# Optimization experiments

Hardware: AMD Instinct MI355X
Metric: run time of the kernel (lower is better)

## Reference

```python
import jax, jax.numpy as jnp
import numpy as np
from jax import lax

DILATIONS = (1, 2, 4)
K = 3        # kernel_size
HORIZON = 6


def _gcn(x, src, dst, W, b, n):
    # PyG GCNConv with self-loops: D^{-1/2}(A+I)D^{-1/2} X W + b
    xw = x @ W                                                # [N,H]
    e = src.shape[0]
    deg = 1.0 + jax.ops.segment_sum(jnp.ones((e,), x.dtype), dst, num_segments=n)
    dinv = lax.rsqrt(deg)                                     # [N]
    msg = xw[src] * (dinv[src] * dinv[dst])[:, None]          # [E,H]
    agg = jax.ops.segment_sum(msg, dst, num_segments=n)       # [N,H]
    return agg + xw * (dinv * dinv)[:, None] + b


def _cell(x, src, dst, win, gcn_w, gcn_b, conv_w, conv_b, proj_w, proj_b):
    n = x.shape[0]
    hg = jax.nn.relu(_gcn(x, src, dst, gcn_w, gcn_b, n))      # [N,H]
    tcn_in = jnp.concatenate([win[:, 1:], hg[:, None]], axis=1)  # [N,K,H]
    hin = jnp.transpose(tcn_in, (0, 2, 1))                    # [N,H,K]
    outs = []
    for i, d in enumerate(DILATIONS):
        p = (K - 1) * d // 2
        y = lax.conv_general_dilated(hin, conv_w[i], (1,), [(p, p)],
                                     rhs_dilation=(d,),
                                     dimension_numbers=('NCH', 'OIH', 'NCH'))
        outs.append(y[:, :, -1] + conv_b[i])                  # last temporal position, [N,H]
    h_new = jnp.concatenate(outs, axis=1) @ proj_w.T + proj_b  # [N,H]
    new_win = jnp.concatenate([win[:, 1:], h_new[:, None]], axis=1)
    return h_new, new_win


def reference(x_seq, edge_index_seq, edge_attr_seq, mask_seq, id_seq,
              gcn_w, gcn_b, conv_w, conv_b, proj_w, proj_b, head_w, head_b):
    T, N, _ = x_seq.shape
    H = gcn_w.shape[1]
    win0 = jnp.zeros((N, K, H), x_seq.dtype)

    def enc_step(win, inp):
        x_t, ei_t = inp
        _, win = _cell(x_t, ei_t[0], ei_t[1], win,
                       gcn_w, gcn_b, conv_w, conv_b, proj_w, proj_b)
        return win, None

    win, _ = lax.scan(enc_step, win0, (x_seq, edge_index_seq))

    src, dst = edge_index_seq[-1, 0], edge_index_seq[-1, 1]

    def dec_step(carry, _):
        win, inp = carry
        h_new, win = _cell(inp, src, dst, win,
                           gcn_w, gcn_b, conv_w, conv_b, proj_w, proj_b)
        y = h_new @ head_w.T + head_b                          # [N,C]
        return (win, y), y

    _, preds = lax.scan(dec_step, (win, x_seq[-1]), None, length=HORIZON)
    return preds  # [horizon, N, out_channels]


def setup_inputs() -> dict:
    T, N, F, E, H, C = 12, 20000, 16, 320000, 128, 16
    key = jax.random.key(0)
    ks = jax.random.split(key, 12)
    return {
        'x_seq': jax.random.normal(ks[0], (T, N, F), jnp.float32),
        'edge_index_seq': jax.random.randint(ks[1], (T, 2, E), 0, N, jnp.int64),
        'edge_attr_seq': jax.random.normal(ks[2], (T, E, 1), jnp.float32),
        'mask_seq': jnp.ones((T, N), jnp.bool_),
        'id_seq': jnp.tile(jnp.arange(N, dtype=jnp.int32)[None], (T, 1)),
        'gcn_w': jax.random.normal(ks[3], (F, H), jnp.float32) * 0.1,
        'gcn_b': jnp.zeros((H,), jnp.float32),
        'conv_w': jax.random.normal(ks[4], (3, H, H, K), jnp.float32) * 0.05,
        'conv_b': jnp.zeros((3, H), jnp.float32),
        'proj_w': jax.random.normal(ks[5], (H, 3 * H), jnp.float32) * 0.05,
        'proj_b': jnp.zeros((H,), jnp.float32),
        'head_w': jax.random.normal(ks[6], (C, H), jnp.float32) * 0.05,
        'head_b': jnp.zeros((C,), jnp.float32),
    }
```

## Files before the change

### kernel.cpp

```cpp
#include <hip/hip_runtime.h>

#define NN 20000
#define NP 20032
#define EE 320000
#define TT 12
#define HH 128
#define FF 16
#define CC 16
#define HOR 6

#define NB 313
#define WPT 84
#define CHE 3812

#define NBLK 79

typedef __attribute__((ext_vector_type(8))) short short8;
typedef __attribute__((ext_vector_type(4))) float f32x4;

__device__ __forceinline__ float blo(unsigned int u) {
    union { float f; unsigned int i; } v; v.i = u << 16; return v.f;
}
__device__ __forceinline__ float bhi(unsigned int u) {
    union { float f; unsigned int i; } v; v.i = u & 0xffff0000u; return v.f;
}
__device__ __forceinline__ unsigned short f2b(float f) {
    union { float f; unsigned int i; } v; v.f = f;
    unsigned int x = v.i;
    return (unsigned short)((x + 0x7fffu + ((x >> 16) & 1u)) >> 16);
}
__device__ __forceinline__ unsigned int pck(float lo, float hi) {
    return ((unsigned int)f2b(hi) << 16) | f2b(lo);
}
__device__ __forceinline__ void addrow(float* acc, uint4 r) {
    acc[0] += blo(r.x); acc[1] += bhi(r.x);
    acc[2] += blo(r.y); acc[3] += bhi(r.y);
    acc[4] += blo(r.z); acc[5] += bhi(r.z);
    acc[6] += blo(r.w); acc[7] += bhi(r.w);
}

__global__ void k_zero(int* p, int n) {
    int i = blockIdx.x * 256 + threadIdx.x;
    if (i < n) p[i] = 0;
}

__global__ __launch_bounds__(512) void k_binA(const int* __restrict__ ei,
                                              int* __restrict__ gData,
                                              int* __restrict__ pcnt,
                                              int* __restrict__ pofs) {
    int wg = blockIdx.x;
    int t = wg / WPT, w = wg - t * WPT;
    __shared__ int lcnt[NB];
    __shared__ int sm[512];
    __shared__ __align__(16) int elist[CHE];
    int tid = threadIdx.x;
    for (int i = tid; i < NB; i += 512) lcnt[i] = 0;
    __syncthreads();
    int e0 = w * CHE, e1 = min(EE, e0 + CHE);
    int total = e1 - e0;
    const int* si = ei + (size_t)t * 2 * EE;
    const int* di = si + EE;
    int eA = e0 + tid * 4, eB = eA + 2048;
    bool hA = eA < e1, hB = eB < e1;
    int sA[4], dA[4], pA[4], sB[4], dB[4], pB[4];
    if (hA) {
        int4 s4 = *(const int4*)(si + eA);
        int4 d4 = *(const int4*)(di + eA);
        sA[0] = s4.x; sA[1] = s4.y; sA[2] = s4.z; sA[3] = s4.w;
        dA[0] = d4.x; dA[1] = d4.y; dA[2] = d4.z; dA[3] = d4.w;
    }
    if (hB) {
        int4 s4 = *(const int4*)(si + eB);
        int4 d4 = *(const int4*)(di + eB);
        sB[0] = s4.x; sB[1] = s4.y; sB[2] = s4.z; sB[3] = s4.w;
        dB[0] = d4.x; dB[1] = d4.y; dB[2] = d4.z; dB[3] = d4.w;
    }
    if (hA) {
#pragma unroll
        for (int k = 0; k < 4; k++) pA[k] = atomicAdd(&lcnt[dA[k] >> 6], 1);
    }
    if (hB) {
#pragma unroll
        for (int k = 0; k < 4; k++) pB[k] = atomicAdd(&lcnt[dB[k] >> 6], 1);
    }
    __syncthreads();
    sm[tid] = (tid < NB) ? lcnt[tid] : 0;
    __syncthreads();
    for (int off = 1; off < 512; off <<= 1) {
        int u = (tid >= off) ? sm[tid - off] : 0;
        __syncthreads();
        sm[tid] += u;
        __syncthreads();
    }
    if (tid < NB) {
        int v = lcnt[tid];
        int ex = sm[tid] - v;
        size_t o = (size_t)(t * WPT + w) * NB + tid;
        pcnt[o] = v;
        pofs[o] = ex;
        sm[tid] = ex;
    }
    __syncthreads();
    if (hA) {
#pragma unroll
        for (int k = 0; k < 4; k++) {
            int b = dA[k] >> 6;
            elist[sm[b] + pA[k]] = ((dA[k] & 63) << 16) | sA[k];
        }
    }
    if (hB) {
#pragma unroll
        for (int k = 0; k < 4; k++) {
            int b = dB[k] >> 6;
            elist[sm[b] + pB[k]] = ((dB[k] & 63) << 16) | sB[k];
        }
    }
    __syncthreads();
    int* gOut = gData + (size_t)(t * WPT + w) * CHE;
    for (int i = tid * 4; i < total; i += 2048)
        *(int4*)(gOut + i) = *(const int4*)&elist[i];
}

__global__ __launch_bounds__(512) void k_bscan2(const int* __restrict__ pcnt,
                                                int* __restrict__ bbase,
                                                int* __restrict__ rowptr) {
    int t = blockIdx.x, tid = threadIdx.x;
    __shared__ int sm[512];
    int v = 0;
    if (tid < NB)
        for (int w = 0; w < WPT; w++) v += pcnt[(size_t)(t * WPT + w) * NB + tid];
    sm[tid] = v;
    __syncthreads();
    for (int off = 1; off < 512; off <<= 1) {
        int u = (tid >= off) ? sm[tid - off] : 0;
        __syncthreads();
        sm[tid] += u;
        __syncthreads();
    }
    if (tid < NB) bbase[t * NB + tid] = sm[tid] - v;
    if (tid == 511) rowptr[(size_t)t * (NN + 1) + NN] = sm[511];
}

__global__ __launch_bounds__(256) void k_placeB(const int* __restrict__ gData,
                                                const int* __restrict__ pcnt,
                                                const int* __restrict__ pofs,
                                                const int* __restrict__ bbase,
                                                int* __restrict__ rowptr,
                                                float* __restrict__ dinv,
                                                unsigned short* __restrict__ csr) {
    int t = blockIdx.x / NB, b = blockIdx.x - t * NB;
    int tid = threadIdx.x;
    __shared__ int scnt[WPT], sofs[WPT], cofs[WPT + 1];
    __shared__ int elist[2048];
    __shared__ int cnt64[64], lofs[64], place[64];
    if (tid < WPT) {
        size_t o = (size_t)(t * WPT + tid) * NB + b;
        scnt[tid] = pcnt[o];
        sofs[tid] = pofs[o];
    }
    if (tid < 64) cnt64[tid] = 0;
    __syncthreads();
    if (tid == 0) {
        int s = 0;
        for (int w = 0; w < WPT; w++) { cofs[w] = s; s += scnt[w]; }
        cofs[WPT] = s;
    }
    __syncthreads();
    int total = cofs[WPT];
    int wv = tid >> 6, lane = tid & 63;
    for (int w = wv; w < WPT; w += 4) {
        int c = scnt[w], o = cofs[w];
        const int* sp = gData + (size_t)(t * WPT + w) * CHE + sofs[w];
        for (int i = lane; i < c; i += 64) elist[o + i] = sp[i];
    }
    __syncthreads();
    for (int i = tid; i < total; i += 256) atomicAdd(&cnt64[elist[i] >> 16], 1);
    __syncthreads();
    if (tid == 0) {
        int s = 0;
        for (int j = 0; j < 64; j++) { lofs[j] = s; place[j] = s; s += cnt64[j]; }
    }
    __syncthreads();
    int base = bbase[t * NB + b];
    int n = b * 64 + tid;
    if (tid < 64 && n < NN) {
        rowptr[(size_t)t * (NN + 1) + n] = base + lofs[tid];
        dinv[(size_t)t * NN + n] = rsqrtf(1.0f + (float)cnt64[tid]);
    }
    unsigned short* cbase = csr + (size_t)t * EE + base;
    for (int i = tid; i < total; i += 256) {
        int en = elist[i];
        int r = atomicAdd(&place[en >> 16], 1);
        cbase[r] = (unsigned short)(en & 0xffff);
    }
}

__global__ void k_count(const int* __restrict__ ei, int* __restrict__ cnt) {
    int idx = blockIdx.x * 256 + threadIdx.x;
    if (idx >= TT * EE) return;
    int t = idx / EE, e = idx - t * EE;
    int d = ei[t * 2 * EE + EE + e];
    atomicAdd(&cnt[t * NN + d], 1);
}

__global__ void k_dinvF(const int* __restrict__ cnt, float* __restrict__ dinv) {
    int idx = blockIdx.x * 256 + threadIdx.x;
    if (idx >= TT * NN) return;
    dinv[idx] = 1.0f / sqrtf(1.0f + (float)cnt[idx]);
}

__global__ void k_scan(const int* __restrict__ cnt, int* __restrict__ rowptr, int* __restrict__ wofs) {
    int t = blockIdx.x;
    const int* c = cnt + t * NN;
    int* rp = rowptr + t * (NN + 1);
    int* wo = wofs + t * NN;
    __shared__ int sums[1024];
    int tid = threadIdx.x;
    const int CH2 = 20;
    int base = tid * CH2;
    int loc[CH2];
    int s = 0;
    for (int i = 0; i < CH2; i++) { int ix = base + i; int v = (ix < NN) ? c[ix] : 0; loc[i] = s; s += v; }
    sums[tid] = s;
    __syncthreads();
    for (int off = 1; off < 1024; off <<= 1) {
        int v = (tid >= off) ? sums[tid - off] : 0;
        __syncthreads();
        sums[tid] += v;
        __syncthreads();
    }
    int excl = (tid > 0) ? sums[tid - 1] : 0;
    for (int i = 0; i < CH2; i++) {
        int ix = base + i;
        if (ix < NN) { int e = excl + loc[i]; rp[ix] = e; wo[ix] = e; }
    }
    if (tid == 1023) rp[NN] = sums[1023];
}

__global__ void k_place(const int* __restrict__ ei, int* __restrict__ wofs,
                        unsigned short* __restrict__ csr) {
    int idx = blockIdx.x * 256 + threadIdx.x;
    if (idx >= TT * EE) return;
    int t = idx / EE, e = idx - t * EE;
    int s = ei[t * 2 * EE + e];
    int d = ei[t * 2 * EE + EE + e];
    int pos = atomicAdd(&wofs[t * NN + d], 1);
    csr[t * EE + pos] = (unsigned short)s;
}

__global__ void k_wprepB(const float* __restrict__ cw, const float* __restrict__ pw,
                         const float* __restrict__ cb, const float* __restrict__ pb,
                         unsigned short* __restrict__ Bpk, float* __restrict__ Bf32,
                         float* __restrict__ bias) {
    int idx = blockIdx.x * 256 + threadIdx.x;
    if (blockIdx.x == 192) {
        int h = threadIdx.x;
        if (h < HH) {
            float m = pb[h];
            for (int d = 0; d < 3; d++)
                for (int o = 0; o < HH; o++)
                    m += cb[d * HH + o] * pw[h * 384 + d * HH + o];
            bias[h] = m;
        }
        return;
    }
    if (idx >= 384 * HH) return;
    int kk = idx / HH, h = idx - kk * HH;
    float m = 0.f;
    if (kk < 128) {
        int i = kk;
        for (int o = 0; o < HH; o++)
            m += cw[((1 * HH + o) * HH + i) * 3 + 0] * pw[h * 384 + 128 + o];
    } else if (kk < 256) {
        int i = kk - 128;
        for (int o = 0; o < HH; o++)
            m += cw[((0 * HH + o) * HH + i) * 3 + 0] * pw[h * 384 + o];
    } else {
        int i = kk - 256;
        for (int d = 0; d < 3; d++)
            for (int o = 0; o < HH; o++)
                m += cw[((d * HH + o) * HH + i) * 3 + 1] * pw[h * 384 + d * HH + o];
    }
    Bf32[kk * HH + h] = m;
    int ki = kk >> 5, r = kk & 31, q = r >> 3, j = r & 7, nt = h >> 4, ln = q * 16 + (h & 15);
    Bpk[(size_t)((ki * 8 + nt) * 64 + ln) * 8 + j] = f2b(m);
}

__global__ __launch_bounds__(256) void k_packP(const float* __restrict__ Bf32,
                                               const float* __restrict__ biasT,
                                               unsigned short* __restrict__ Bpk2,
                                               float* __restrict__ biasP) {
    int gidx = blockIdx.x * 256 + threadIdx.x;
    if (gidx < 16 * 16 * 64 * 8) {
        int j = gidx & 7, ln = (gidx >> 3) & 63, nt = (gidx >> 9) & 15, kb = gidx >> 13;
        int q = ln >> 4;
        int kk = (kb & 3) * 32 + q * 8 + j;
        int c = nt * 16 + (ln & 15);
        int s = c >> 7, h = c & 127;
        int g = kb >> 2;
        const float* M2 = Bf32;
        const float* M1 = Bf32 + 128 * HH;
        const float* Mh = Bf32 + 256 * HH;
        float v = 0.f;
        if (g == 0) {
            if (s == 0) v = M2[kk * HH + h];
            else { for (int o = 0; o < HH; o++) v += M2[kk * HH + o] * M1[o * HH + h]; }
        } else if (g == 1) {
            if (s == 0) v = M1[kk * HH + h];
            else {
                v = M2[kk * HH + h];
                for (int o = 0; o < HH; o++) v += M1[kk * HH + o] * M1[o * HH + h];
            }
        } else if (g == 2) {
            if (s == 0) v = Mh[kk * HH + h];
            else { for (int o = 0; o < HH; o++) v += Mh[kk * HH + o] * M1[o * HH + h]; }
        } else {
            v = (s == 0) ? 0.f : Mh[kk * HH + h];
        }
        Bpk2[gidx] = f2b(v);
    } else if (gidx < 16 * 16 * 64 * 8 + 256) {
        int c = gidx - 16 * 16 * 64 * 8;
        if (c < 128) biasP[c] = biasT[c];
        else {
            int h = c & 127;
            float v = biasT[h];
            const float* M1 = Bf32 + 128 * HH;
            for (int o = 0; o < HH; o++) v += biasT[o] * M1[o * HH + h];
            biasP[c] = v;
        }
    }
}

__global__ void k_xs(const float* __restrict__ x, const float* __restrict__ dinv,
                     unsigned short* __restrict__ xs) {
    int idx = blockIdx.x * 256 + threadIdx.x;
    if (idx >= TT * NN) return;
    float dn = dinv[idx];
    const float4* xr = (const float4*)(x + (size_t)idx * FF);
    unsigned int res[8];
#pragma unroll
    for (int k = 0; k < 4; k++) {
        float4 v = xr[k];
        res[2 * k]     = pck(v.x * dn, v.y * dn);
        res[2 * k + 1] = pck(v.z * dn, v.w * dn);
    }
    uint4* dst = (uint4*)(xs + (size_t)idx * FF);
    dst[0] = *(uint4*)(res);
    dst[1] = *(uint4*)(res + 4);
}

__global__ __launch_bounds__(256) void k_aggX(const unsigned short* __restrict__ xsA,
                                              const unsigned short* __restrict__ csrA,
                                              const int* __restrict__ rpA,
                                              const float* __restrict__ dinvA,
                                              float* __restrict__ zA) {
    int b = blockIdx.x;
    int g = b / NBLK, nb = b - g * NBLK;
    int n = nb * 256 + threadIdx.x;
    if (n >= NN) return;
    const unsigned short* xs = xsA + (size_t)g * NN * FF;
    const unsigned short* csr = csrA + (size_t)g * EE;
    const int* rp = rpA + (size_t)g * (NN + 1);
    float acc[16];
    {
        const uint4* sp = (const uint4*)(xs + (size_t)n * FF);
        uint4 a = sp[0], b4 = sp[1];
        acc[0] = blo(a.x);  acc[1] = bhi(a.x);  acc[2] = blo(a.y);  acc[3] = bhi(a.y);
        acc[4] = blo(a.z);  acc[5] = bhi(a.z);  acc[6] = blo(a.w);  acc[7] = bhi(a.w);
        acc[8] = blo(b4.x); acc[9] = bhi(b4.x); acc[10] = blo(b4.y); acc[11] = bhi(b4.y);
        acc[12] = blo(b4.z); acc[13] = bhi(b4.z); acc[14] = blo(b4.w); acc[15] = bhi(b4.w);
    }
    int j0 = rp[n], j1 = rp[n + 1];
    int j = j0;
    for (; j + 1 < j1; j += 2) {
        int s0 = csr[j], s1 = csr[j + 1];
        const uint4* p0 = (const uint4*)(xs + (size_t)s0 * FF);
        const uint4* p1 = (const uint4*)(xs + (size_t)s1 * FF);
        uint4 a0 = p0[0], a1 = p0[1], b0 = p1[0], b1 = p1[1];
        addrow(acc, a0); addrow(acc + 8, a1);
        addrow(acc, b0); addrow(acc + 8, b1);
    }
    if (j < j1) {
        const uint4* p0 = (const uint4*)(xs + (size_t)csr[j] * FF);
        uint4 a0 = p0[0], a1 = p0[1];
        addrow(acc, a0); addrow(acc + 8, a1);
    }
    float dn = dinvA[(size_t)g * NN + n];
    float4* zo = (float4*)(zA + (size_t)g * NP * FF + (size_t)n * FF);
#pragma unroll
    for (int k = 0; k < 4; k++)
        zo[k] = make_float4(acc[4 * k] * dn, acc[4 * k + 1] * dn,
                            acc[4 * k + 2] * dn, acc[4 * k + 3] * dn);
}

__device__ __forceinline__ void hg_frag(const float* zsh, const float* Wg, const float* gbs,
                                        int mr, int q, short8* hgf) {
    float zr[16];
    {
        const float4* zp = (const float4*)(zsh + mr * FF);
        float4 z0 = zp[0], z1 = zp[1], z2 = zp[2], z3 = zp[3];
        zr[0] = z0.x; zr[1] = z0.y; zr[2] = z0.z; zr[3] = z0.w;
        zr[4] = z1.x; zr[5] = z1.y; zr[6] = z1.z; zr[7] = z1.w;
        zr[8] = z2.x; zr[9] = z2.y; zr[10] = z2.z; zr[11] = z2.w;
        zr[12] = z3.x; zr[13] = z3.y; zr[14] = z3.z; zr[15] = z3.w;
    }
#pragma unroll
    for (int k2 = 0; k2 < 4; k2++) {
        float s[8];
#pragma unroll
        for (int c = 0; c < 8; c++) s[c] = gbs[k2 * 32 + q * 8 + c];
#pragma unroll
        for (int f = 0; f < 16; f++) {
            const float4* wp = (const float4*)(Wg + f * HH + k2 * 32 + q * 8);
            float4 w0 = wp[0], w1 = wp[1];
            float zf = zr[f];
            s[0] += zf * w0.x; s[1] += zf * w0.y; s[2] += zf * w0.z; s[3] += zf * w0.w;
            s[4] += zf * w1.x; s[5] += zf * w1.y; s[6] += zf * w1.z; s[7] += zf * w1.w;
        }
#pragma unroll
        for (int c = 0; c < 8; c++) hgf[k2][c] = (short)f2b(fmaxf(s[c], 0.f));
    }
}

__global__ __launch_bounds__(256, 4) void k_gemm2(const unsigned short* __restrict__ a0,
                                                  const unsigned short* __restrict__ a1,
                                                  const float* __restrict__ zA,
                                                  const float* __restrict__ zB,
                                                  const float* __restrict__ gw,
                                                  const float* __restrict__ gb,
                                                  const unsigned short* __restrict__ Bpk2,
                                                  const float* __restrict__ biasP,
                                                  unsigned short* __restrict__ out0,
                                                  unsigned short* __restrict__ out1) {
    __shared__ float Wg[FF * HH];
    __shared__ float zshA[16 * FF], zshB[16 * FF];
    __shared__ float gbs[HH];
    __shared__ float bps[256];
    __shared__ __align__(16) unsigned short hgA[16 * 136], hgB[16 * 136];
    __shared__ __align__(16) unsigned short csh[16 * 264];
    int tid = threadIdx.x;
    int wid = tid >> 6, lane = tid & 63;
    int m0b = blockIdx.x * 16;
    int mr = lane & 15, q = lane >> 4;
    for (int i = tid; i < FF * HH; i += 256) Wg[i] = gw[i];
    if (tid < 16 * FF) {
        zshA[tid] = zA[(size_t)m0b * FF + tid];
        zshB[tid] = zB[(size_t)m0b * FF + tid];
    }
    if (tid < HH) gbs[tid] = gb[tid];
    bps[tid] = biasP[tid];
    __syncthreads();
    if (wid == 0) {
        short8 hgf[4];
        hg_frag(zshA, Wg, gbs, mr, q, hgf);
#pragma unroll
        for (int k2 = 0; k2 < 4; k2++)
            *(short8*)&hgA[mr * 136 + k2 * 32 + q * 8] = hgf[k2];
    } else if (wid == 1) {
        short8 hgf[4];
        hg_frag(zshB, Wg, gbs, mr, q, hgf);
#pragma unroll
        for (int k2 = 0; k2 < 4; k2++)
            *(short8*)&hgB[mr * 136 + k2 * 32 + q * 8] = hgf[k2];
    }
    __syncthreads();
    int nt0 = wid * 4;
    f32x4 acc[4];
#pragma unroll
    for (int j = 0; j < 4; j++) acc[j] = (f32x4){0.f, 0.f, 0.f, 0.f};
#pragma unroll
    for (int kb = 0; kb < 12; kb++) {
        short8 bf[4];
#pragma unroll
        for (int j = 0; j < 4; j++)
            bf[j] = *(const short8*)(Bpk2 + (size_t)((kb * 16 + nt0 + j) * 64 + lane) * 8);
        short8 af;
        if (kb < 4)
            af = *(const short8*)(a0 + (size_t)(m0b + mr) * HH + kb * 32 + q * 8);
        else if (kb < 8)
            af = *(const short8*)(a1 + (size_t)(m0b + mr) * HH + (kb - 4) * 32 + q * 8);
        else
            af = *(const short8*)&hgA[mr * 136 + (kb - 8) * 32 + q * 8];
#pragma unroll
        for (int j = 0; j < 4; j++)
            acc[j] = __builtin_amdgcn_mfma_f32_16x16x32_bf16(af, bf[j], acc[j], 0, 0, 0);
    }
    if (wid >= 2) {
#pragma unroll
        for (int k2 = 0; k2 < 4; k2++) {
            int kb = 12 + k2;
            short8 bf[4];
#pragma unroll
            for (int j = 0; j < 4; j++)
                bf[j] = *(const short8*)(Bpk2 + (size_t)((kb * 16 + nt0 + j) * 64 + lane) * 8);
            short8 af = *(const short8*)&hgB[mr * 136 + k2 * 32 + q * 8];
#pragma unroll
            for (int j = 0; j < 4; j++)
                acc[j] = __builtin_amdgcn_mfma_f32_16x16x32_bf16(af, bf[j], acc[j], 0, 0, 0);
        }
    }
#pragma unroll
    for (int j = 0; j < 4; j++) {
        int c = (nt0 + j) * 16 + mr;
        float bv = bps[c];
#pragma unroll
        for (int r = 0; r < 4; r++)
            csh[(q * 4 + r) * 264 + c] = f2b(acc[j][r] + bv);
    }
    __syncthreads();
#pragma unroll
    for (int i = 0; i < 2; i++) {
        int idx = i * 256 + tid;
        int row = idx >> 5, c8 = (idx & 31) * 8;
        short8 v = *(const short8*)&csh[row * 264 + c8];
        if (c8 < 128) *(short8*)(out0 + (size_t)(m0b + row) * HH + c8) = v;
        else          *(short8*)(out1 + (size_t)(m0b + row) * HH + (c8 - 128)) = v;
    }
}

__global__ __launch_bounds__(256, 3) void k_gemmF2(const unsigned short* __restrict__ a0,
                                                   const unsigned short* __restrict__ a1,
                                                   const float* __restrict__ zt, int gather,
                                                   const float* __restrict__ gw,
                                                   const float* __restrict__ gb,
                                                   const unsigned short* __restrict__ Bpk,
                                                   const float* __restrict__ bias,
                                                   unsigned short* __restrict__ out,
                                                   const float* __restrict__ hw,
                                                   const float* __restrict__ hbv,
                                                   const float* __restrict__ dinvN,
                                                   const int* __restrict__ rp,
                                                   const unsigned short* __restrict__ csr,
                                                   unsigned short* __restrict__ xsD,
                                                   float* __restrict__ yout) {
    __shared__ float Wg[FF * HH];
    __shared__ float Whs[CC * 132];
    __shared__ float gbs[HH], biasS[HH], hbS[CC];
    __shared__ float zsh[16 * FF];
    __shared__ __align__(16) unsigned short hgD[16 * 136];
    __shared__ unsigned short hsh[16 * 136];
    __shared__ float ysh[16 * 17];
    int tid = threadIdx.x;
    int wid = tid >> 6, lane = tid & 63;
    int m0b = blockIdx.x * 16;
    int mr = lane & 15, q = lane >> 4;
    for (int i = tid; i < FF * HH; i += 256) {
        Wg[i] = gw[i];
        Whs[(i >> 7) * 132 + (i & 127)] = hw[i];
    }
    if (tid < HH) { gbs[tid] = gb[tid]; biasS[tid] = bias[tid]; }
    if (tid < CC) hbS[tid] = hbv[tid];
    if (!gather) {
        if (tid < 16 * FF) zsh[tid] = zt[(size_t)m0b * FF + tid];
    } else {
        int r = tid >> 4, p = tid & 15, half = p & 1, eo = p >> 1;
        int n = m0b + r;
        float a[8];
#pragma unroll
        for (int k = 0; k < 8; k++) a[k] = 0.f;
        if (n < NN) {
            int j0 = rp[n], j1 = rp[n + 1];
            for (int j = j0 + eo; j < j1; j += 8) {
                int s = csr[j];
                uint4 v = *(const uint4*)(xsD + (size_t)s * FF + half * 8);
                addrow(a, v);
            }
        }
#pragma unroll
        for (int k = 0; k < 8; k++) {
            a[k] += __shfl_xor(a[k], 2);
            a[k] += __shfl_xor(a[k], 4);
            a[k] += __shfl_xor(a[k], 8);
        }
        if (n < NN && eo == 0) {
            uint4 sv = *(const uint4*)(xsD + (size_t)n * FF + half * 8);
            addrow(a, sv);
            float dn = dinvN[n];
#pragma unroll
            for (int k = 0; k < 8; k++) zsh[r * FF + half * 8 + k] = a[k] * dn;
        }
    }
    __syncthreads();
    if (wid == 0) {
        short8 hgf[4];
        hg_frag(zsh, Wg, gbs, mr, q, hgf);
#pragma unroll
        for (int k2 = 0; k2 < 4; k2++)
            *(short8*)&hgD[mr * 136 + k2 * 32 + q * 8] = hgf[k2];
    }
    __syncthreads();
    int nt0 = wid * 2;
    f32x4 acc[2];
#pragma unroll
    for (int j = 0; j < 2; j++) acc[j] = (f32x4){0.f, 0.f, 0.f, 0.f};
#pragma unroll
    for (int ki = 0; ki < 12; ki++) {
        short8 bf[2];
#pragma unroll
        for (int j = 0; j < 2; j++)
            bf[j] = *(const short8*)(Bpk + (size_t)((ki * 8 + nt0 + j) * 64 + lane) * 8);
        short8 af;
        if (ki < 4)
            af = *(const short8*)(a0 + (size_t)(m0b + mr) * HH + ki * 32 + q * 8);
        else if (ki < 8)
            af = *(const short8*)(a1 + (size_t)(m0b + mr) * HH + (ki - 4) * 32 + q * 8);
        else
            af = *(const short8*)&hgD[mr * 136 + (ki - 8) * 32 + q * 8];
#pragma unroll
        for (int j = 0; j < 2; j++)
            acc[j] = __builtin_amdgcn_mfma_f32_16x16x32_bf16(af, bf[j], acc[j], 0, 0, 0);
    }
#pragma unroll
    for (int j = 0; j < 2; j++) {
        int feat = (nt0 + j) * 16 + mr;
        float bv = biasS[feat];
#pragma unroll
        for (int r = 0; r < 4; r++)
            hsh[(q * 4 + r) * 136 + feat] = f2b(acc[j][r] + bv);
    }
    __syncthreads();
    {
        int row = tid >> 4, c8 = (tid & 15) * 8;
        *(short8*)(out + (size_t)(m0b + row) * HH + c8) =
            *(const short8*)&hsh[row * 136 + c8];
    }
    {
        int r = tid >> 4, c = tid & 15;
        float y = hbS[c];
        for (int k = 0; k < HH; k++)
            y += blo((unsigned int)hsh[r * 136 + k]) * Whs[c * 132 + k];
        ysh[r * 17 + c] = y;
        int gn = m0b + r;
        if (gn < NN) yout[(size_t)gn * CC + c] = y;
    }
    __syncthreads();
    if (tid < 16) {
        int gn = m0b + tid;
        if (gn < NN) {
            float dn = dinvN[gn];
            unsigned int res[8];
#pragma unroll
            for (int k = 0; k < 8; k++)
                res[k] = pck(ysh[tid * 17 + 2 * k] * dn, ysh[tid * 17 + 2 * k + 1] * dn);
            uint4* dst = (uint4*)(xsD + (size_t)gn * FF);
            dst[0] = *(uint4*)(res);
            dst[1] = *(uint4*)(res + 4);
        }
    }
}

extern "C" void kernel_launch(void* const* d_in, const int* in_sizes, int n_in,
                              void* d_out, int out_size, void* d_ws, size_t ws_size,
                              hipStream_t stream) {
    const float* x_seq  = (const float*)d_in[0];
    const int*   ei     = (const int*)d_in[1];
    const float* gcn_w  = (const float*)d_in[5];
    const float* gcn_b  = (const float*)d_in[6];
    const float* conv_w = (const float*)d_in[7];
    const float* conv_b = (const float*)d_in[8];
    const float* proj_w = (const float*)d_in[9];
    const float* proj_b = (const float*)d_in[10];
    const float* head_w = (const float*)d_in[11];
    const float* head_b = (const float*)d_in[12];
    float* outp = (float*)d_out;

    char* ws = (char*)d_ws;
    size_t off = 0;
    auto alloc = [&](size_t bytes) { void* p = ws + off; off += (bytes + 255) & ~(size_t)255; return p; };
    float*          dinv   = (float*)alloc((size_t)TT * NN * 4);
    int*            rowptr = (int*)alloc((size_t)TT * (NN + 1) * 4);
    unsigned short* csr    = (unsigned short*)alloc((size_t)TT * EE * 2);
    unsigned short* hb0    = (unsigned short*)alloc((size_t)NP * HH * 2);
    unsigned short* hb1    = (unsigned short*)alloc((size_t)NP * HH * 2);
    unsigned short* hb2    = (unsigned short*)alloc((size_t)NP * HH * 2);
    unsigned short* hb3    = (unsigned short*)alloc((size_t)NP * HH * 2);
    unsigned short* xsD    = (unsigned short*)alloc((size_t)NP * FF * 2);
    unsigned short* Bpk    = (unsigned short*)alloc((size_t)384 * HH * 2);
    float*          Bf32   = (float*)alloc((size_t)384 * HH * 4);
    float*          biasT  = (float*)alloc(HH * 4);
    unsigned short* Bpk2   = (unsigned short*)alloc((size_t)16 * 16 * 64 * 8 * 2);
    float*          biasP  = (float*)alloc(256 * 4);
    size_t tb = off;
    unsigned short* xs12 = (unsigned short*)alloc((size_t)TT * NN * FF * 2);
    float*          z12  = (float*)alloc((size_t)TT * NP * FF * 4);
    size_t compute_end = off;
    off = tb;
    int* gData = (int*)alloc((size_t)TT * WPT * CHE * 4);
    int* pcnt  = (int*)alloc((size_t)TT * WPT * NB * 4);
    int* pofs  = (int*)alloc((size_t)TT * WPT * NB * 4);
    int* bbase = (int*)alloc((size_t)TT * NB * 4);
    size_t csr_end = off;
    bool fastcsr = (csr_end <= ws_size && compute_end <= ws_size);

    k_zero<<<(NP * HH + 255) / 256, 256, 0, stream>>>((int*)hb2, NP * HH);

    if (fastcsr) {
        k_binA<<<TT * WPT, 512, 0, stream>>>(ei, gData, pcnt, pofs);
        k_bscan2<<<TT, 512, 0, stream>>>(pcnt, bbase, rowptr);
        k_placeB<<<TT * NB, 256, 0, stream>>>(gData, pcnt, pofs, bbase, rowptr, dinv, csr);
    } else {
        off = tb;
        int* cnt  = (int*)alloc((size_t)TT * NN * 4);
        int* wofs = (int*)alloc((size_t)TT * NN * 4);
        k_zero<<<(TT * NN + 255) / 256, 256, 0, stream>>>(cnt, TT * NN);
        k_count<<<(TT * EE + 255) / 256, 256, 0, stream>>>(ei, cnt);
        k_dinvF<<<(TT * NN + 255) / 256, 256, 0, stream>>>(cnt, dinv);
        k_scan<<<TT, 1024, 0, stream>>>(cnt, rowptr, wofs);
        k_place<<<(TT * EE + 255) / 256, 256, 0, stream>>>(ei, wofs, csr);
    }

    k_wprepB<<<193, 256, 0, stream>>>(conv_w, proj_w, conv_b, proj_b, Bpk, Bf32, biasT);
    k_packP<<<(16 * 16 * 64 * 8 + 256 + 255) / 256, 256, 0, stream>>>(Bf32, biasT, Bpk2, biasP);

    k_xs<<<(TT * NN + 255) / 256, 256, 0, stream>>>(x_seq, dinv, xs12);
    k_aggX<<<TT * NBLK, 256, 0, stream>>>(xs12, csr, rowptr, dinv, z12);

    unsigned short* hbuf[4] = {hb0, hb1, hb2, hb3};
    for (int t = 0; t < TT; t += 2) {
        k_gemm2<<<NP / 16, 256, 0, stream>>>(hbuf[(t + 2) & 3], hbuf[(t + 3) & 3],
                                             z12 + (size_t)t * NP * FF,
                                             z12 + (size_t)(t + 1) * NP * FF,
                                             gcn_w, gcn_b, Bpk2, biasP,
                                             hbuf[t & 3], hbuf[(t + 1) & 3]);
    }
    const float* dinv11 = dinv + (size_t)(TT - 1) * NN;
    const int* rp11 = rowptr + (size_t)(TT - 1) * (NN + 1);
    const unsigned short* csr11 = csr + (size_t)(TT - 1) * EE;
    for (int t = TT; t < TT + HOR; t++) {
        const float* zt = (t == TT) ? (z12 + (size_t)(TT - 1) * NP * FF) : nullptr;
        k_gemmF2<<<NP / 16, 256, 0, stream>>>(hbuf[(t + 2) & 3], hbuf[(t + 3) & 3],
                                              zt, (t == TT) ? 0 : 1,
                                              gcn_w, gcn_b, Bpk, biasT, hbuf[t & 3],
                                              head_w, head_b, dinv11, rp11, csr11,
                                              xsD, outp + (size_t)(t - TT) * NN * CC);
    }
}
```

Measured before the change: 489.9 us.

## Split aggX edge gather across thread pairs and group graphs per XCD

```diff
diff --git a/kernel.cpp b/kernel.cpp
--- a/kernel.cpp
+++ b/kernel.cpp
@@ -13,7 +13,7 @@
 #define WPT 84
 #define CHE 3812
 
-#define NBLK 79
+#define AGG_GRID 1896
 
 typedef __attribute__((ext_vector_type(8))) short short8;
 typedef __attribute__((ext_vector_type(4))) float f32x4;
@@ -354,26 +354,25 @@
                                               const int* __restrict__ rpA,
                                               const float* __restrict__ dinvA,
                                               float* __restrict__ zA) {
-    int b = blockIdx.x;
-    int g = b / NBLK, nb = b - g * NBLK;
-    int n = nb * 256 + threadIdx.x;
+    int bid = blockIdx.x;
+    int x = bid & 7, k = bid >> 3;
+    int h = 3 * x + k / 79;
+    int g = h >> 1;
+    int nb = (h & 1) * 79 + (k % 79);
+    int tid = threadIdx.x;
+    int r = tid >> 1, eo = tid & 1;
+    int n = nb * 128 + r;
     if (n >= NN) return;
     const unsigned short* xs = xsA + (size_t)g * NN * FF;
     const unsigned short* csr = csrA + (size_t)g * EE;
     const int* rp = rpA + (size_t)g * (NN + 1);
     float acc[16];
-    {
-        const uint4* sp = (const uint4*)(xs + (size_t)n * FF);
-        uint4 a = sp[0], b4 = sp[1];
-        acc[0] = blo(a.x);  acc[1] = bhi(a.x);  acc[2] = blo(a.y);  acc[3] = bhi(a.y);
-        acc[4] = blo(a.z);  acc[5] = bhi(a.z);  acc[6] = blo(a.w);  acc[7] = bhi(a.w);
-        acc[8] = blo(b4.x); acc[9] = bhi(b4.x); acc[10] = blo(b4.y); acc[11] = bhi(b4.y);
-        acc[12] = blo(b4.z); acc[13] = bhi(b4.z); acc[14] = blo(b4.w); acc[15] = bhi(b4.w);
-    }
+#pragma unroll
+    for (int i = 0; i < 16; i++) acc[i] = 0.f;
     int j0 = rp[n], j1 = rp[n + 1];
-    int j = j0;
-    for (; j + 1 < j1; j += 2) {
-        int s0 = csr[j], s1 = csr[j + 1];
+    int j = j0 + eo;
+    for (; j + 2 < j1; j += 4) {
+        int s0 = csr[j], s1 = csr[j + 2];
         const uint4* p0 = (const uint4*)(xs + (size_t)s0 * FF);
         const uint4* p1 = (const uint4*)(xs + (size_t)s1 * FF);
         uint4 a0 = p0[0], a1 = p0[1], b0 = p1[0], b1 = p1[1];
@@ -385,12 +384,19 @@
         uint4 a0 = p0[0], a1 = p0[1];
         addrow(acc, a0); addrow(acc + 8, a1);
     }
-    float dn = dinvA[(size_t)g * NN + n];
-    float4* zo = (float4*)(zA + (size_t)g * NP * FF + (size_t)n * FF);
-#pragma unroll
-    for (int k = 0; k < 4; k++)
-        zo[k] = make_float4(acc[4 * k] * dn, acc[4 * k + 1] * dn,
-                            acc[4 * k + 2] * dn, acc[4 * k + 3] * dn);
+#pragma unroll
+    for (int i = 0; i < 16; i++) acc[i] += __shfl_xor(acc[i], 1);
+    if (eo == 0) {
+        const uint4* sp = (const uint4*)(xs + (size_t)n * FF);
+        uint4 a = sp[0], b4 = sp[1];
+        addrow(acc, a); addrow(acc + 8, b4);
+        float dn = dinvA[(size_t)g * NN + n];
+        float4* zo = (float4*)(zA + (size_t)g * NP * FF + (size_t)n * FF);
+#pragma unroll
+        for (int k2 = 0; k2 < 4; k2++)
+            zo[k2] = make_float4(acc[4 * k2] * dn, acc[4 * k2 + 1] * dn,
+                                 acc[4 * k2 + 2] * dn, acc[4 * k2 + 3] * dn);
+    }
 }
 
 __device__ __forceinline__ void hg_frag(const float* zsh, const float* Wg, const float* gbs,
@@ -713,7 +719,7 @@
     k_packP<<<(16 * 16 * 64 * 8 + 256 + 255) / 256, 256, 0, stream>>>(Bf32, biasT, Bpk2, biasP);
 
     k_xs<<<(TT * NN + 255) / 256, 256, 0, stream>>>(x_seq, dinv, xs12);
-    k_aggX<<<TT * NBLK, 256, 0, stream>>>(xs12, csr, rowptr, dinv, z12);
+    k_aggX<<<AGG_GRID, 256, 0, stream>>>(xs12, csr, rowptr, dinv, z12);
 
     unsigned short* hbuf[4] = {hb0, hb1, hb2, hb3};
     for (int t = 0; t < TT; t += 2) {
```

New measurement: 468.7 us. -4.3%, faster.
